# Optimization experiments

Measured on AMD Instinct MI355X. Metric: run time of the kernel, lower is better.

The kernel has to match this reference:

```python
import jax, jax.numpy as jnp
import numpy as np


def conv1x1(x, w, bias):
    # x: [B,C,H,W], w: [O,C], bias: [O]
    return jnp.einsum('bchw,oc->bohw', x, w) + bias[None, :, None, None]


def setup_inputs() -> dict:
    key = jax.random.key(0)
    ks = jax.random.split(key, 12)
    B, Cin_half, H, W = 8, 128, 128, 128
    Cin, Cout = 256, 256
    s_in = 1.0 / np.sqrt(Cin)
    s_out = 1.0 / np.sqrt(Cout)
    return {
        'a': jax.random.normal(ks[0], (B, Cin_half, H, W), jnp.float32),
        'b': jax.random.normal(ks[1], (B, Cin_half, H, W), jnp.float32),
        'w1': jax.random.uniform(ks[2], (Cout, Cin), jnp.float32, -s_in, s_in),
        'b1': jax.random.uniform(ks[3], (Cout,), jnp.float32, -s_in, s_in),
        'w2': jax.random.uniform(ks[4], (Cout, Cout), jnp.float32, -s_out, s_out),
        'b2': jax.random.uniform(ks[5], (Cout,), jnp.float32, -s_out, s_out),
        'w3': jax.random.uniform(ks[6], (Cout, Cout), jnp.float32, -s_out, s_out),
        'b3': jax.random.uniform(ks[7], (Cout,), jnp.float32, -s_out, s_out),
        'w4': jax.random.uniform(ks[8], (Cout, Cout), jnp.float32, -s_out, s_out),
        'b4': jax.random.uniform(ks[9], (Cout,), jnp.float32, -s_out, s_out),
    }


def reference(a, b, w1, b1, w2, b2, w3, b3, w4, b4):
    z = jnp.concatenate([a, b], axis=1)            # [B, Cin, H, W]
    z = conv1x1(z, w1, b1)                          # [B, C, H, W]
    B, C, H, W = z.shape
    q = conv1x1(z, w2, b2).reshape(B, C, H * W)     # [B, C, N]
    k = conv1x1(z, w3, b3).reshape(B, C, H * W)
    v = conv1x1(z, w4, b4).reshape(B, C, H * W)
    qk = jnp.einsum('bcn,bdn->bcd', q, k)           # [B, C, C] (q @ k^T)
    attn = jax.nn.softmax(qk, axis=-1)
    out = jnp.einsum('bcd,bdn->bcn', attn, v)       # [B, C, N]
    return out.reshape(B, C, H, W)
```

## Files before the change

kernel.cpp:

```cpp
#include <hip/hip_runtime.h>

typedef float  f4v  __attribute__((ext_vector_type(4)));
typedef __bf16 bf8v __attribute__((ext_vector_type(8)));
typedef unsigned int u32x2 __attribute__((ext_vector_type(2)));
typedef unsigned int u32x4 __attribute__((ext_vector_type(4)));
typedef unsigned short u16;

#define MFMA(a,b,c) __builtin_amdgcn_mfma_f32_16x16x32_bf16((a),(b),(c),0,0,0)
#define HW_N 16384

__device__ __forceinline__ u16 bf_rne(float x){
  unsigned u = __float_as_uint(x);
  u += 0x7fffu + ((u >> 16) & 1u);
  return (u16)(u >> 16);
}

__global__ void k_weights(const float* __restrict__ w1, const float* __restrict__ b1,
                          const float* __restrict__ w2, const float* __restrict__ b2,
                          const float* __restrict__ w3, const float* __restrict__ b3,
                          const float* __restrict__ w4, const float* __restrict__ b4,
                          float* __restrict__ Wq, float* __restrict__ WkT,
                          float* __restrict__ Wv, float* __restrict__ bq,
                          float* __restrict__ bk, float* __restrict__ bv)
{
  const int blk = blockIdx.x, t = threadIdx.x;
  if (blk == 96){
    float aq = 0.f, ak = 0.f, av = 0.f;
    for (int j = 0; j < 256; ++j){
      const float bb = b1[j];
      aq += w2[t*256 + j] * bb;
      ak += w3[t*256 + j] * bb;
      av += w4[t*256 + j] * bb;
    }
    bq[t] = aq + b2[t];
    bk[t] = ak + b3[t];
    bv[t] = av + b4[t];
    return;
  }
  for (int i = 0; i < 8; ++i){
    const int e   = blk*2048 + i*256 + t;
    const int mat = e >> 16;
    const int c   = (e >> 8) & 255;
    const int col = e & 255;
    const float* wsrc = (mat == 0) ? w2 : ((mat == 1) ? w3 : w4);
    float acc = 0.f;
    for (int j = 0; j < 256; ++j) acc += wsrc[c*256 + j] * w1[j*256 + col];
    if      (mat == 0) Wq [c*256 + col] = acc;
    else if (mat == 1) WkT[col*256 + c] = acc;
    else               Wv [c*256 + col] = acc;
  }
}

__global__ __launch_bounds__(512, 2) void k_gram(
    const float* __restrict__ xa, const float* __restrict__ xb,
    float* __restrict__ Gpart, float* __restrict__ spart)
{
  __shared__ u16 hbuf[2][256*64];
  __shared__ u16 lbuf[2][256*64];
  const int blk = blockIdx.x;
  const int b = blk >> 5, half = (blk >> 4) & 1, chunk = blk & 15;
  const int t = threadIdx.x;
  const int lane = t & 63, w = t >> 6;
  const int wr = w >> 1, wc = w & 1;
  const int c4 = t & 15, crow = t >> 4;

  const float* rowp[8];
#pragma unroll
  for (int p = 0; p < 8; ++p){
    const int c = crow + 32*p;
    const float* base = (c < 128) ? (xa + (size_t)(b*128 + c) * HW_N)
                                  : (xb + (size_t)(b*128 + (c-128)) * HW_N);
    rowp[p] = base + c4*4;
  }

  float ssum[8];
#pragma unroll
  for (int p = 0; p < 8; ++p) ssum[p] = 0.f;

  const f4v vzero = {0.f, 0.f, 0.f, 0.f};
  f4v acc[4][4];
#pragma unroll
  for (int i = 0; i < 4; ++i)
#pragma unroll
    for (int j = 0; j < 4; ++j) acc[i][j] = vzero;

  f4v ld[8];
  auto issue = [&](int s){
    const int n0 = chunk*1024 + s*64;
#pragma unroll
    for (int p = 0; p < 8; ++p) ld[p] = *(const f4v*)(rowp[p] + n0);
  };
  auto wbuf = [&](int bi){
#pragma unroll
    for (int p = 0; p < 8; ++p){
      const int c = crow + 32*p;
      const f4v v = ld[p];
      ssum[p] += (v[0] + v[1]) + (v[2] + v[3]);
      u16 h[4], l[4];
#pragma unroll
      for (int i = 0; i < 4; ++i){
        const float x = v[i];
        const u16 hb = bf_rne(x);
        const float hf = __uint_as_float(((unsigned)hb) << 16);
        h[i] = hb; l[i] = bf_rne(x - hf);
      }
      u32x2 hp, lp;
      hp[0] = (unsigned)h[0] | ((unsigned)h[1] << 16);
      hp[1] = (unsigned)h[2] | ((unsigned)h[3] << 16);
      lp[0] = (unsigned)l[0] | ((unsigned)l[1] << 16);
      lp[1] = (unsigned)l[2] | ((unsigned)l[3] << 16);
      const int off = c*64 + (((c4 >> 1) ^ (c & 7)) * 8) + (c4 & 1) * 4;
      *(u32x2*)&hbuf[bi][off] = hp;
      *(u32x2*)&lbuf[bi][off] = lp;
    }
  };
  auto mstep = [&](int bi){
#pragma unroll
    for (int kk = 0; kk < 2; ++kk){
      bf8v ah[4], al[4], bh[4], bl[4];
#pragma unroll
      for (int f = 0; f < 4; ++f){
        const int so = kk*4 + (lane >> 4);
        const int r  = wr*64 + f*16 + (lane & 15);
        const int oa = r*64 + ((so ^ (r & 7)) * 8);
        ah[f] = *(const bf8v*)&hbuf[bi][oa];
        al[f] = *(const bf8v*)&lbuf[bi][oa];
        const int rc = 128*half + wc*64 + f*16 + (lane & 15);
        const int ob = rc*64 + ((so ^ (rc & 7)) * 8);
        bh[f] = *(const bf8v*)&hbuf[bi][ob];
        bl[f] = *(const bf8v*)&lbuf[bi][ob];
      }
#pragma unroll
      for (int i = 0; i < 4; ++i)
#pragma unroll
        for (int j = 0; j < 4; ++j){
          acc[i][j] = MFMA(ah[i], bh[j], acc[i][j]);
          acc[i][j] = MFMA(ah[i], bl[j], acc[i][j]);
          acc[i][j] = MFMA(al[i], bh[j], acc[i][j]);
        }
    }
  };

  issue(0); wbuf(0); __syncthreads();
  for (int s = 0; s < 16; ++s){
    const int cur = s & 1;
    if (s < 15) issue(s + 1);
    mstep(cur);
    if (s < 15) wbuf(cur ^ 1);
    __syncthreads();
  }

  float* gp = Gpart + (size_t)((b*2 + half)*16 + chunk) * 32768;
#pragma unroll
  for (int i = 0; i < 4; ++i)
#pragma unroll
    for (int j = 0; j < 4; ++j){
      const int row = wr*64 + i*16 + ((lane >> 4) << 2);
      const int col = wc*64 + j*16 + (lane & 15);
#pragma unroll
      for (int r2 = 0; r2 < 4; ++r2)
        gp[(row + r2)*128 + col] = acc[i][j][r2];
    }

  if (half == 0){
#pragma unroll
    for (int p = 0; p < 8; ++p){
      float v = ssum[p];
      v += __shfl_xor(v, 1);
      v += __shfl_xor(v, 2);
      v += __shfl_xor(v, 4);
      v += __shfl_xor(v, 8);
      if ((lane & 15) == 0)
        spart[(b*16 + chunk)*256 + (crow + 32*p)] = v;
    }
  }
}

__global__ void k_redg(const float* __restrict__ Gpart, float* __restrict__ G)
{
  for (int k = 0; k < 8; ++k){
    const int o = blockIdx.x*2048 + k*256 + threadIdx.x;
    const int b = o >> 16, r = (o >> 8) & 255, col = o & 255;
    const int half = col >> 7, cc = col & 127;
    const float* p = Gpart + (size_t)(b*2 + half)*524288 + (size_t)r*128 + cc;
    float s = 0.f;
#pragma unroll
    for (int ch = 0; ch < 16; ++ch) s += p[ch*32768];
    G[o] = s;
  }
}

__device__ __forceinline__ float block_red(float v, int ismax, volatile float* red, int t){
#pragma unroll
  for (int m = 32; m; m >>= 1){
    const float o = __shfl_xor(v, m);
    v = ismax ? fmaxf(v, o) : (v + o);
  }
  if ((t & 63) == 0) red[t >> 6] = v;
  __syncthreads();
  const float r01 = ismax ? fmaxf(red[0], red[1]) : (red[0] + red[1]);
  const float r23 = ismax ? fmaxf(red[2], red[3]) : (red[2] + red[3]);
  v = ismax ? fmaxf(r01, r23) : (r01 + r23);
  __syncthreads();
  return v;
}

__global__ __launch_bounds__(256, 2) void k_attn(
    const float* __restrict__ G, const float* __restrict__ spart,
    const float* __restrict__ Wq, const float* __restrict__ WkT,
    const float* __restrict__ Wv, const float* __restrict__ bq,
    const float* __restrict__ bk, const float* __restrict__ bv,
    u16* __restrict__ Mfrag, float* __restrict__ cb)
{
  __shared__ float s_lds[256];
  __shared__ float wq_lds[4][256];
  __shared__ float t1_lds[4][256];
  __shared__ float a_lds[4][256];
  __shared__ float red[4];
  const int blk = blockIdx.x;
  const int b = blk >> 6, r0 = (blk & 63) * 4;
  const int t = threadIdx.x;

  float sv = 0.f;
#pragma unroll
  for (int ch = 0; ch < 16; ++ch) sv += spart[(b*16 + ch)*256 + t];
  s_lds[t] = sv;
#pragma unroll
  for (int ri = 0; ri < 4; ++ri) wq_lds[ri][t] = Wq[(r0 + ri)*256 + t];
  __syncthreads();

  float t1[4] = {0,0,0,0}, pv[4] = {0,0,0,0};
  const float* gb = G + (size_t)b * 65536;
  for (int k = 0; k < 256; ++k){
    const float g  = gb[k*256 + t];
    const float sk = s_lds[k];
#pragma unroll
    for (int ri = 0; ri < 4; ++ri){
      const float wqv = wq_lds[ri][k];
      t1[ri] += wqv * g;
      pv[ri] += wqv * sk;
    }
  }
#pragma unroll
  for (int ri = 0; ri < 4; ++ri) t1_lds[ri][t] = t1[ri];
  __syncthreads();

  float qk[4] = {0,0,0,0}, rd = 0.f;
  for (int n = 0; n < 256; ++n){
    const float wkt = WkT[n*256 + t];
    rd += wkt * s_lds[n];
#pragma unroll
    for (int ri = 0; ri < 4; ++ri) qk[ri] += t1_lds[ri][n] * wkt;
  }
  const float bkv = bk[t];
#pragma unroll
  for (int ri = 0; ri < 4; ++ri){
    const float bqv = bq[r0 + ri];
    qk[ri] += pv[ri]*bkv + bqv*rd + 16384.f*bqv*bkv;
  }

  float areg[4];
#pragma unroll
  for (int ri = 0; ri < 4; ++ri){
    const float m = block_red(qk[ri], 1, red, t);
    const float e = __expf(qk[ri] - m);
    const float s = block_red(e, 0, red, t);
    areg[ri] = e / s;
    a_lds[ri][t] = areg[ri];
  }
  const float bvv = bv[t];
#pragma unroll
  for (int ri = 0; ri < 4; ++ri){
    const float c = block_red(areg[ri]*bvv, 0, red, t);
    if (t == 0) cb[b*256 + r0 + ri] = c;
  }
  __syncthreads();

  float m4[4] = {0,0,0,0};
  for (int d = 0; d < 256; ++d){
    const float wv = Wv[d*256 + t];
#pragma unroll
    for (int ri = 0; ri < 4; ++ri) m4[ri] += a_lds[ri][d] * wv;
  }
  const int ks = t >> 5, lhi = (t >> 3) & 3, j = t & 7;
#pragma unroll
  for (int ri = 0; ri < 4; ++ri){
    const int o = r0 + ri;
    Mfrag[(size_t)b*65536 +
          (size_t)((((o >> 4)*8 + ks)*64) + (o & 15) + (lhi << 4))*8 + j] = bf_rne(m4[ri]);
  }
}

__global__ __launch_bounds__(512, 4) void k_out(
    const float* __restrict__ xa, const float* __restrict__ xb,
    const u16* __restrict__ Mfrag, const float* __restrict__ cb,
    float* __restrict__ out)
{
  __shared__ u16 xt[2][32*256];
  const int blk = blockIdx.x;
  const int b = blk >> 6, nchunk = blk & 63;
  const int t = threadIdx.x;
  const int lane = t & 63, w = t >> 6;
  const int cr = t >> 1;
  const int hf = t & 1;

  const float* rowbase = (cr < 128) ? (xa + (size_t)(b*128 + cr)*HW_N)
                                    : (xb + (size_t)(b*128 + (cr-128))*HW_N);
  const float* rp = rowbase + hf*16;

  f4v ld[4];
  auto issue = [&](int s){
    const int n0 = nchunk*256 + s*32;
#pragma unroll
    for (int q = 0; q < 4; ++q) ld[q] = *(const f4v*)(rp + n0 + q*4);
  };
  auto cvtwrite = [&](int bi){
#pragma unroll
    for (int q = 0; q < 4; ++q){
      const f4v v = ld[q];
#pragma unroll
      for (int i = 0; i < 4; ++i){
        const int n = hf*16 + q*4 + i;
        xt[bi][n*256 + (((cr >> 3) ^ (n & 15))*8) + (cr & 7)] = bf_rne(v[i]);
      }
    }
  };

  issue(0);

  u32x4 af[2][8];
  const u16* mb = Mfrag + (size_t)b * 65536;
#pragma unroll
  for (int f = 0; f < 2; ++f)
#pragma unroll
    for (int ks = 0; ks < 8; ++ks)
      af[f][ks] = *(const u32x4*)(mb + (size_t)((((w*2 + f)*8 + ks)*64 + lane))*8);
#pragma unroll
  for (int f = 0; f < 2; ++f)
#pragma unroll
    for (int ks = 0; ks < 8; ++ks)
      asm volatile("" : "+a"(af[f][ks]));

  float cbv[2];
#pragma unroll
  for (int f = 0; f < 2; ++f)
    cbv[f] = cb[b*256 + w*32 + f*16 + (lane & 15)];

  const f4v vzero = {0.f, 0.f, 0.f, 0.f};
  float* outp = out + (size_t)b*256*HW_N;

  cvtwrite(0);
  __syncthreads();

  for (int s = 0; s < 8; ++s){
    const int cur = s & 1;
    if (s < 7) issue(s + 1);

    const int n0 = nchunk*256 + s*32;
    f4v acc[2][2];
#pragma unroll
    for (int f = 0; f < 2; ++f){ acc[f][0] = vzero; acc[f][1] = vzero; }

#pragma unroll
    for (int ks = 0; ks < 8; ++ks){
      bf8v xf[2];
#pragma unroll
      for (int g = 0; g < 2; ++g){
        const int n  = g*16 + (lane & 15);
        const int so = ks*4 + (lane >> 4);
        xf[g] = *(const bf8v*)&xt[cur][n*256 + ((so ^ (n & 15))*8)];
      }
#pragma unroll
      for (int f = 0; f < 2; ++f){
        acc[f][0] = MFMA(xf[0], __builtin_bit_cast(bf8v, af[f][ks]), acc[f][0]);
        acc[f][1] = MFMA(xf[1], __builtin_bit_cast(bf8v, af[f][ks]), acc[f][1]);
      }
    }

#pragma unroll
    for (int f = 0; f < 2; ++f){
      const int row = w*32 + f*16 + (lane & 15);
#pragma unroll
      for (int g = 0; g < 2; ++g){
        const int px = n0 + g*16 + ((lane >> 4) << 2);
        f4v v = acc[f][g] + cbv[f];
        *(f4v*)&outp[(size_t)row*HW_N + px] = v;
      }
    }

    if (s < 7) cvtwrite(cur ^ 1);
    __syncthreads();
  }
}

extern "C" void kernel_launch(void* const* d_in, const int* in_sizes, int n_in,
                              void* d_out, int out_size, void* d_ws, size_t ws_size,
                              hipStream_t stream)
{
  const float* xa = (const float*)d_in[0];
  const float* xb = (const float*)d_in[1];
  const float* w1 = (const float*)d_in[2];
  const float* b1 = (const float*)d_in[3];
  const float* w2 = (const float*)d_in[4];
  const float* b2 = (const float*)d_in[5];
  const float* w3 = (const float*)d_in[6];
  const float* b3 = (const float*)d_in[7];
  const float* w4 = (const float*)d_in[8];
  const float* b4 = (const float*)d_in[9];
  float* out = (float*)d_out;
  char*  ws  = (char*)d_ws;

  float* Gpart = (float*)(ws + 0);
  float* G     = (float*)(ws + 33554432);
  float* spart = (float*)(ws + 35651584);
  float* Wq    = (float*)(ws + 35782656);
  float* WkT   = (float*)(ws + 36044800);
  float* Wv    = (float*)(ws + 36306944);
  float* bq    = (float*)(ws + 36569088);
  float* bk    = (float*)(ws + 36570112);
  float* bv    = (float*)(ws + 36571136);
  u16*   Mfrag = (u16*)  (ws + 36572160);
  float* cb    = (float*)(ws + 37620736);

  hipLaunchKernelGGL(k_weights, dim3(97),  dim3(256), 0, stream,
                     w1,b1,w2,b2,w3,b3,w4,b4, Wq,WkT,Wv,bq,bk,bv);
  hipLaunchKernelGGL(k_gram,    dim3(256), dim3(512), 0, stream, xa, xb, Gpart, spart);
  hipLaunchKernelGGL(k_redg,    dim3(256), dim3(256), 0, stream, Gpart, G);
  hipLaunchKernelGGL(k_attn,    dim3(512), dim3(256), 0, stream,
                     G, spart, Wq, WkT, Wv, bq, bk, bv, Mfrag, cb);
  hipLaunchKernelGGL(k_out,     dim3(512), dim3(512), 0, stream, xa, xb, Mfrag, cb, out);
}
```

Before: 257.4 us.

## Compute full Gram per block with atomic reduction and cache bf16 input copy

k_gram now has each block compute the full 256x256 Gram tile over a shorter spatial chunk instead of a half-tile. Partial results go into G through atomicAdd, which removes the Gpart buffer and the k_redg reduction kernel. The same pass writes a bf16 copy of the input, so k_out reads half the bytes and skips the float-to-bf16 conversion. The cost is 8x4 accumulator tiles per wave, which raises register pressure, atomic contention on G, an extra memset, and an extra 64MB bf16 write in the gram pass.

```diff
diff --git a/kernel.cpp b/kernel.cpp
--- a/kernel.cpp
+++ b/kernel.cpp
@@ -5,6 +5,7 @@
 typedef unsigned int u32x2 __attribute__((ext_vector_type(2)));
 typedef unsigned int u32x4 __attribute__((ext_vector_type(4)));
 typedef unsigned short u16;
+typedef unsigned short u16x8 __attribute__((ext_vector_type(8)));
 
 #define MFMA(a,b,c) __builtin_amdgcn_mfma_f32_16x16x32_bf16((a),(b),(c),0,0,0)
 #define HW_N 16384
@@ -53,44 +54,44 @@
 
 __global__ __launch_bounds__(512, 2) void k_gram(
     const float* __restrict__ xa, const float* __restrict__ xb,
-    float* __restrict__ Gpart, float* __restrict__ spart)
+    float* __restrict__ G, float* __restrict__ spart,
+    u16* __restrict__ xbf)
 {
   __shared__ u16 hbuf[2][256*64];
   __shared__ u16 lbuf[2][256*64];
   const int blk = blockIdx.x;
-  const int b = blk >> 5, half = (blk >> 4) & 1, chunk = blk & 15;
+  const int b = blk >> 5, chunk = blk & 31;
   const int t = threadIdx.x;
   const int lane = t & 63, w = t >> 6;
-  const int wr = w >> 1, wc = w & 1;
+  const int wr = w >> 2, wc = w & 3;
   const int c4 = t & 15, crow = t >> 4;
 
-  const float* rowp[8];
-#pragma unroll
-  for (int p = 0; p < 8; ++p){
-    const int c = crow + 32*p;
-    const float* base = (c < 128) ? (xa + (size_t)(b*128 + c) * HW_N)
-                                  : (xb + (size_t)(b*128 + (c-128)) * HW_N);
-    rowp[p] = base + c4*4;
-  }
+  const float* xpa = xa + (((size_t)(b*128) + crow) << 14) + c4*4;
+  const float* xpb = xb + (((size_t)(b*128) + crow) << 14) + c4*4;
+  u16*        xpo = xbf + (((size_t)(b*256) + crow) << 14) + c4*4;
 
   float ssum[8];
 #pragma unroll
   for (int p = 0; p < 8; ++p) ssum[p] = 0.f;
 
   const f4v vzero = {0.f, 0.f, 0.f, 0.f};
-  f4v acc[4][4];
-#pragma unroll
-  for (int i = 0; i < 4; ++i)
-#pragma unroll
-    for (int j = 0; j < 4; ++j) acc[i][j] = vzero;
+  f4v acc[8][4];
+#pragma unroll
+  for (int f = 0; f < 8; ++f)
+#pragma unroll
+    for (int j = 0; j < 4; ++j) acc[f][j] = vzero;
 
   f4v ld[8];
   auto issue = [&](int s){
-    const int n0 = chunk*1024 + s*64;
-#pragma unroll
-    for (int p = 0; p < 8; ++p) ld[p] = *(const f4v*)(rowp[p] + n0);
+    const size_t n0 = (size_t)chunk*512 + s*64;
+#pragma unroll
+    for (int p = 0; p < 8; ++p){
+      const float* src = (p < 4) ? (xpa + ((size_t)p << 19)) : (xpb + ((size_t)(p-4) << 19));
+      ld[p] = *(const f4v*)(src + n0);
+    }
   };
-  auto wbuf = [&](int bi){
+  auto wbuf = [&](int bi, int s){
+    const size_t n0 = (size_t)chunk*512 + s*64;
 #pragma unroll
     for (int p = 0; p < 8; ++p){
       const int c = crow + 32*p;
@@ -101,8 +102,8 @@
       for (int i = 0; i < 4; ++i){
         const float x = v[i];
         const u16 hb = bf_rne(x);
-        const float hf = __uint_as_float(((unsigned)hb) << 16);
-        h[i] = hb; l[i] = bf_rne(x - hf);
+        const float hfv = __uint_as_float(((unsigned)hb) << 16);
+        h[i] = hb; l[i] = bf_rne(x - hfv);
       }
       u32x2 hp, lp;
       hp[0] = (unsigned)h[0] | ((unsigned)h[1] << 16);
@@ -112,81 +113,67 @@
       const int off = c*64 + (((c4 >> 1) ^ (c & 7)) * 8) + (c4 & 1) * 4;
       *(u32x2*)&hbuf[bi][off] = hp;
       *(u32x2*)&lbuf[bi][off] = lp;
+      *(u32x2*)(xpo + ((size_t)p << 19) + n0) = hp;
     }
   };
   auto mstep = [&](int bi){
 #pragma unroll
     for (int kk = 0; kk < 2; ++kk){
-      bf8v ah[4], al[4], bh[4], bl[4];
-#pragma unroll
-      for (int f = 0; f < 4; ++f){
-        const int so = kk*4 + (lane >> 4);
-        const int r  = wr*64 + f*16 + (lane & 15);
+      const int so = kk*4 + (lane >> 4);
+      bf8v bh[4], bl[4];
+#pragma unroll
+      for (int g = 0; g < 4; ++g){
+        const int rc = wc*64 + g*16 + (lane & 15);
+        const int ob = rc*64 + ((so ^ (rc & 7)) * 8);
+        bh[g] = *(const bf8v*)&hbuf[bi][ob];
+        bl[g] = *(const bf8v*)&lbuf[bi][ob];
+      }
+#pragma unroll
+      for (int f = 0; f < 8; ++f){
+        const int r  = wr*128 + f*16 + (lane & 15);
         const int oa = r*64 + ((so ^ (r & 7)) * 8);
-        ah[f] = *(const bf8v*)&hbuf[bi][oa];
-        al[f] = *(const bf8v*)&lbuf[bi][oa];
-        const int rc = 128*half + wc*64 + f*16 + (lane & 15);
-        const int ob = rc*64 + ((so ^ (rc & 7)) * 8);
-        bh[f] = *(const bf8v*)&hbuf[bi][ob];
-        bl[f] = *(const bf8v*)&lbuf[bi][ob];
-      }
-#pragma unroll
-      for (int i = 0; i < 4; ++i)
+        const bf8v ah = *(const bf8v*)&hbuf[bi][oa];
+        const bf8v al = *(const bf8v*)&lbuf[bi][oa];
 #pragma unroll
         for (int j = 0; j < 4; ++j){
-          acc[i][j] = MFMA(ah[i], bh[j], acc[i][j]);
-          acc[i][j] = MFMA(ah[i], bl[j], acc[i][j]);
-          acc[i][j] = MFMA(al[i], bh[j], acc[i][j]);
+          acc[f][j] = MFMA(ah, bh[j], acc[f][j]);
+          acc[f][j] = MFMA(ah, bl[j], acc[f][j]);
+          acc[f][j] = MFMA(al, bh[j], acc[f][j]);
         }
+      }
     }
   };
 
-  issue(0); wbuf(0); __syncthreads();
-  for (int s = 0; s < 16; ++s){
+  issue(0); wbuf(0, 0); __syncthreads();
+  for (int s = 0; s < 8; ++s){
     const int cur = s & 1;
-    if (s < 15) issue(s + 1);
+    if (s < 7) issue(s + 1);
     mstep(cur);
-    if (s < 15) wbuf(cur ^ 1);
+    if (s < 7) wbuf(cur ^ 1, s + 1);
     __syncthreads();
   }
 
-  float* gp = Gpart + (size_t)((b*2 + half)*16 + chunk) * 32768;
-#pragma unroll
-  for (int i = 0; i < 4; ++i)
+  float* gb = G + (size_t)b * 65536;
+#pragma unroll
+  for (int f = 0; f < 8; ++f)
 #pragma unroll
     for (int j = 0; j < 4; ++j){
-      const int row = wr*64 + i*16 + ((lane >> 4) << 2);
+      const int row = wr*128 + f*16 + ((lane >> 4) << 2);
       const int col = wc*64 + j*16 + (lane & 15);
 #pragma unroll
       for (int r2 = 0; r2 < 4; ++r2)
-        gp[(row + r2)*128 + col] = acc[i][j][r2];
-    }
-
-  if (half == 0){
-#pragma unroll
-    for (int p = 0; p < 8; ++p){
-      float v = ssum[p];
-      v += __shfl_xor(v, 1);
-      v += __shfl_xor(v, 2);
-      v += __shfl_xor(v, 4);
-      v += __shfl_xor(v, 8);
-      if ((lane & 15) == 0)
-        spart[(b*16 + chunk)*256 + (crow + 32*p)] = v;
-    }
-  }
-}
-
-__global__ void k_redg(const float* __restrict__ Gpart, float* __restrict__ G)
-{
-  for (int k = 0; k < 8; ++k){
-    const int o = blockIdx.x*2048 + k*256 + threadIdx.x;
-    const int b = o >> 16, r = (o >> 8) & 255, col = o & 255;
-    const int half = col >> 7, cc = col & 127;
-    const float* p = Gpart + (size_t)(b*2 + half)*524288 + (size_t)r*128 + cc;
-    float s = 0.f;
-#pragma unroll
-    for (int ch = 0; ch < 16; ++ch) s += p[ch*32768];
-    G[o] = s;
+        atomicAdd(&gb[(size_t)(row + r2)*256 + col], acc[f][j][r2]);
+    }
+
+#pragma unroll
+  for (int p = 0; p < 8; ++p){
+    float v = ssum[p];
+    v += __shfl_xor(v, 1);
+    v += __shfl_xor(v, 2);
+    v += __shfl_xor(v, 4);
+    v += __shfl_xor(v, 8);
+    if ((lane & 15) == 0)
+      spart[(b*32 + chunk)*256 + (crow + 32*p)] = v;
   }
 }
 
@@ -223,7 +210,7 @@
 
   float sv = 0.f;
 #pragma unroll
-  for (int ch = 0; ch < 16; ++ch) sv += spart[(b*16 + ch)*256 + t];
+  for (int ch = 0; ch < 32; ++ch) sv += spart[(b*32 + ch)*256 + t];
   s_lds[t] = sv;
 #pragma unroll
   for (int ri = 0; ri < 4; ++ri) wq_lds[ri][t] = Wq[(r0 + ri)*256 + t];
@@ -292,9 +279,8 @@
 }
 
 __global__ __launch_bounds__(512, 4) void k_out(
-    const float* __restrict__ xa, const float* __restrict__ xb,
-    const u16* __restrict__ Mfrag, const float* __restrict__ cb,
-    float* __restrict__ out)
+    const u16* __restrict__ xbf, const u16* __restrict__ Mfrag,
+    const float* __restrict__ cb, float* __restrict__ out)
 {
   __shared__ u16 xt[2][32*256];
   const int blk = blockIdx.x;
@@ -304,24 +290,20 @@
   const int cr = t >> 1;
   const int hf = t & 1;
 
-  const float* rowbase = (cr < 128) ? (xa + (size_t)(b*128 + cr)*HW_N)
-                                    : (xb + (size_t)(b*128 + (cr-128))*HW_N);
-  const float* rp = rowbase + hf*16;
-
-  f4v ld[4];
+  const u16* xp = xbf + (((size_t)(b*256) + cr) << 14) + nchunk*256 + hf*16;
+
+  u16x8 ld[2];
   auto issue = [&](int s){
-    const int n0 = nchunk*256 + s*32;
-#pragma unroll
-    for (int q = 0; q < 4; ++q) ld[q] = *(const f4v*)(rp + n0 + q*4);
+#pragma unroll
+    for (int q = 0; q < 2; ++q) ld[q] = *(const u16x8*)(xp + s*32 + q*8);
   };
-  auto cvtwrite = [&](int bi){
-#pragma unroll
-    for (int q = 0; q < 4; ++q){
-      const f4v v = ld[q];
-#pragma unroll
-      for (int i = 0; i < 4; ++i){
-        const int n = hf*16 + q*4 + i;
-        xt[bi][n*256 + (((cr >> 3) ^ (n & 15))*8) + (cr & 7)] = bf_rne(v[i]);
+  auto swrite = [&](int bi){
+#pragma unroll
+    for (int q = 0; q < 2; ++q){
+#pragma unroll
+      for (int j = 0; j < 8; ++j){
+        const int n = hf*16 + q*8 + j;
+        xt[bi][n*256 + (((cr >> 3) ^ (n & 15))*8) + (cr & 7)] = ld[q][j];
       }
     }
   };
@@ -349,7 +331,7 @@
   const f4v vzero = {0.f, 0.f, 0.f, 0.f};
   float* outp = out + (size_t)b*256*HW_N;
 
-  cvtwrite(0);
+  swrite(0);
   __syncthreads();
 
   for (int s = 0; s < 8; ++s){
@@ -388,7 +370,7 @@
       }
     }
 
-    if (s < 7) cvtwrite(cur ^ 1);
+    if (s < 7) swrite(cur ^ 1);
     __syncthreads();
   }
 }
@@ -410,23 +392,25 @@
   float* out = (float*)d_out;
   char*  ws  = (char*)d_ws;
 
-  float* Gpart = (float*)(ws + 0);
-  float* G     = (float*)(ws + 33554432);
-  float* spart = (float*)(ws + 35651584);
-  float* Wq    = (float*)(ws + 35782656);
-  float* WkT   = (float*)(ws + 36044800);
-  float* Wv    = (float*)(ws + 36306944);
-  float* bq    = (float*)(ws + 36569088);
-  float* bk    = (float*)(ws + 36570112);
-  float* bv    = (float*)(ws + 36571136);
-  u16*   Mfrag = (u16*)  (ws + 36572160);
-  float* cb    = (float*)(ws + 37620736);
-
+  float* G     = (float*)(ws + 0);
+  float* spart = (float*)(ws + 2097152);
+  float* Wq    = (float*)(ws + 2359296);
+  float* WkT   = (float*)(ws + 2621440);
+  float* Wv    = (float*)(ws + 2883584);
+  float* bq    = (float*)(ws + 3145728);
+  float* bk    = (float*)(ws + 3146752);
+  float* bv    = (float*)(ws + 3147776);
+  u16*   Mfrag = (u16*)  (ws + 3148800);
+  float* cb    = (float*)(ws + 4197376);
+  u16*   xbf   = (u16*)  (ws + 4205568);
+
+  hipMemsetAsync(G, 0, 2097152, stream);
   hipLaunchKernelGGL(k_weights, dim3(97),  dim3(256), 0, stream,
                      w1,b1,w2,b2,w3,b3,w4,b4, Wq,WkT,Wv,bq,bk,bv);
-  hipLaunchKernelGGL(k_gram,    dim3(256), dim3(512), 0, stream, xa, xb, Gpart, spart);
-  hipLaunchKernelGGL(k_redg,    dim3(256), dim3(256), 0, stream, Gpart, G);
+  hipLaunchKernelGGL(k_gram,    dim3(256), dim3(512), 0, stream,
+                     xa, xb, G, spart, xbf);
   hipLaunchKernelGGL(k_attn,    dim3(512), dim3(256), 0, stream,
                      G, spart, Wq, WkT, Wv, bq, bk, bv, Mfrag, cb);
-  hipLaunchKernelGGL(k_out,     dim3(512), dim3(512), 0, stream, xa, xb, Mfrag, cb, out);
-}
+  hipLaunchKernelGGL(k_out,     dim3(512), dim3(512), 0, stream,
+                     xbf, Mfrag, cb, out);
+}
```

New measurement: 296.5 us. 15.2% more time.

## Atomically reduce Gram partials and cache bf16 input copy for output GEMM

Applied to the files above, without the earlier changes.

The Gram kernel now accumulates its per-chunk partial results straight into G with float atomics, which removes the 32 MB partial buffer and the separate reduction kernel; G is zeroed with a memset first. The half-0 blocks of the Gram kernel also write a bf16-rounded copy of the concatenated input to workspace. The output kernel then reads that bf16 copy (half the bytes) instead of re-reading and converting the fp32 inputs. The cost is extra global writes in k_gram, heavy atomic contention (16 chunks adding into each G element), and a summation order that is no longer deterministic.

```diff
diff --git a/kernel.cpp b/kernel.cpp
--- a/kernel.cpp
+++ b/kernel.cpp
@@ -5,6 +5,7 @@
 typedef unsigned int u32x2 __attribute__((ext_vector_type(2)));
 typedef unsigned int u32x4 __attribute__((ext_vector_type(4)));
 typedef unsigned short u16;
+typedef unsigned short u16x8 __attribute__((ext_vector_type(8)));
 
 #define MFMA(a,b,c) __builtin_amdgcn_mfma_f32_16x16x32_bf16((a),(b),(c),0,0,0)
 #define HW_N 16384
@@ -53,7 +54,8 @@
 
 __global__ __launch_bounds__(512, 2) void k_gram(
     const float* __restrict__ xa, const float* __restrict__ xb,
-    float* __restrict__ Gpart, float* __restrict__ spart)
+    float* __restrict__ G, float* __restrict__ spart,
+    u16* __restrict__ xbf)
 {
   __shared__ u16 hbuf[2][256*64];
   __shared__ u16 lbuf[2][256*64];
@@ -90,7 +92,7 @@
 #pragma unroll
     for (int p = 0; p < 8; ++p) ld[p] = *(const f4v*)(rowp[p] + n0);
   };
-  auto wbuf = [&](int bi){
+  auto wbuf = [&](int bi, int s){
 #pragma unroll
     for (int p = 0; p < 8; ++p){
       const int c = crow + 32*p;
@@ -112,6 +114,9 @@
       const int off = c*64 + (((c4 >> 1) ^ (c & 7)) * 8) + (c4 & 1) * 4;
       *(u32x2*)&hbuf[bi][off] = hp;
       *(u32x2*)&lbuf[bi][off] = lp;
+      if (half == 0){
+        *(u32x2*)&xbf[(size_t)(b*256 + c)*HW_N + chunk*1024 + s*64 + c4*4] = hp;
+      }
     }
   };
   auto mstep = [&](int bi){
@@ -141,25 +146,25 @@
     }
   };
 
-  issue(0); wbuf(0); __syncthreads();
+  issue(0); wbuf(0, 0); __syncthreads();
   for (int s = 0; s < 16; ++s){
     const int cur = s & 1;
     if (s < 15) issue(s + 1);
     mstep(cur);
-    if (s < 15) wbuf(cur ^ 1);
+    if (s < 15) wbuf(cur ^ 1, s + 1);
     __syncthreads();
   }
 
-  float* gp = Gpart + (size_t)((b*2 + half)*16 + chunk) * 32768;
+  float* gb = G + (size_t)b * 65536;
 #pragma unroll
   for (int i = 0; i < 4; ++i)
 #pragma unroll
     for (int j = 0; j < 4; ++j){
       const int row = wr*64 + i*16 + ((lane >> 4) << 2);
-      const int col = wc*64 + j*16 + (lane & 15);
+      const int col = 128*half + wc*64 + j*16 + (lane & 15);
 #pragma unroll
       for (int r2 = 0; r2 < 4; ++r2)
-        gp[(row + r2)*128 + col] = acc[i][j][r2];
+        atomicAdd(&gb[(size_t)(row + r2)*256 + col], acc[i][j][r2]);
     }
 
   if (half == 0){
@@ -173,20 +178,6 @@
       if ((lane & 15) == 0)
         spart[(b*16 + chunk)*256 + (crow + 32*p)] = v;
     }
-  }
-}
-
-__global__ void k_redg(const float* __restrict__ Gpart, float* __restrict__ G)
-{
-  for (int k = 0; k < 8; ++k){
-    const int o = blockIdx.x*2048 + k*256 + threadIdx.x;
-    const int b = o >> 16, r = (o >> 8) & 255, col = o & 255;
-    const int half = col >> 7, cc = col & 127;
-    const float* p = Gpart + (size_t)(b*2 + half)*524288 + (size_t)r*128 + cc;
-    float s = 0.f;
-#pragma unroll
-    for (int ch = 0; ch < 16; ++ch) s += p[ch*32768];
-    G[o] = s;
   }
 }
 
@@ -292,9 +283,8 @@
 }
 
 __global__ __launch_bounds__(512, 4) void k_out(
-    const float* __restrict__ xa, const float* __restrict__ xb,
-    const u16* __restrict__ Mfrag, const float* __restrict__ cb,
-    float* __restrict__ out)
+    const u16* __restrict__ xbf, const u16* __restrict__ Mfrag,
+    const float* __restrict__ cb, float* __restrict__ out)
 {
   __shared__ u16 xt[2][32*256];
   const int blk = blockIdx.x;
@@ -304,24 +294,20 @@
   const int cr = t >> 1;
   const int hf = t & 1;
 
-  const float* rowbase = (cr < 128) ? (xa + (size_t)(b*128 + cr)*HW_N)
-                                    : (xb + (size_t)(b*128 + (cr-128))*HW_N);
-  const float* rp = rowbase + hf*16;
-
-  f4v ld[4];
+  const u16* xp = xbf + (((size_t)(b*256) + cr) << 14) + nchunk*256 + hf*16;
+
+  u16x8 ld[2];
   auto issue = [&](int s){
-    const int n0 = nchunk*256 + s*32;
-#pragma unroll
-    for (int q = 0; q < 4; ++q) ld[q] = *(const f4v*)(rp + n0 + q*4);
+#pragma unroll
+    for (int q = 0; q < 2; ++q) ld[q] = *(const u16x8*)(xp + s*32 + q*8);
   };
-  auto cvtwrite = [&](int bi){
-#pragma unroll
-    for (int q = 0; q < 4; ++q){
-      const f4v v = ld[q];
-#pragma unroll
-      for (int i = 0; i < 4; ++i){
-        const int n = hf*16 + q*4 + i;
-        xt[bi][n*256 + (((cr >> 3) ^ (n & 15))*8) + (cr & 7)] = bf_rne(v[i]);
+  auto swrite = [&](int bi){
+#pragma unroll
+    for (int q = 0; q < 2; ++q){
+#pragma unroll
+      for (int j = 0; j < 8; ++j){
+        const int n = hf*16 + q*8 + j;
+        xt[bi][n*256 + (((cr >> 3) ^ (n & 15))*8) + (cr & 7)] = ld[q][j];
       }
     }
   };
@@ -349,7 +335,7 @@
   const f4v vzero = {0.f, 0.f, 0.f, 0.f};
   float* outp = out + (size_t)b*256*HW_N;
 
-  cvtwrite(0);
+  swrite(0);
   __syncthreads();
 
   for (int s = 0; s < 8; ++s){
@@ -388,7 +374,7 @@
       }
     }
 
-    if (s < 7) cvtwrite(cur ^ 1);
+    if (s < 7) swrite(cur ^ 1);
     __syncthreads();
   }
 }
@@ -410,23 +396,25 @@
   float* out = (float*)d_out;
   char*  ws  = (char*)d_ws;
 
-  float* Gpart = (float*)(ws + 0);
-  float* G     = (float*)(ws + 33554432);
-  float* spart = (float*)(ws + 35651584);
-  float* Wq    = (float*)(ws + 35782656);
-  float* WkT   = (float*)(ws + 36044800);
-  float* Wv    = (float*)(ws + 36306944);
-  float* bq    = (float*)(ws + 36569088);
-  float* bk    = (float*)(ws + 36570112);
-  float* bv    = (float*)(ws + 36571136);
-  u16*   Mfrag = (u16*)  (ws + 36572160);
-  float* cb    = (float*)(ws + 37620736);
-
+  float* G     = (float*)(ws + 0);
+  float* spart = (float*)(ws + 2097152);
+  float* Wq    = (float*)(ws + 2228224);
+  float* WkT   = (float*)(ws + 2490368);
+  float* Wv    = (float*)(ws + 2752512);
+  float* bq    = (float*)(ws + 3014656);
+  float* bk    = (float*)(ws + 3015680);
+  float* bv    = (float*)(ws + 3016704);
+  u16*   Mfrag = (u16*)  (ws + 3017728);
+  float* cb    = (float*)(ws + 4066304);
+  u16*   xbf   = (u16*)  (ws + 4074496);
+
+  hipMemsetAsync(G, 0, 2097152, stream);
   hipLaunchKernelGGL(k_weights, dim3(97),  dim3(256), 0, stream,
                      w1,b1,w2,b2,w3,b3,w4,b4, Wq,WkT,Wv,bq,bk,bv);
-  hipLaunchKernelGGL(k_gram,    dim3(256), dim3(512), 0, stream, xa, xb, Gpart, spart);
-  hipLaunchKernelGGL(k_redg,    dim3(256), dim3(256), 0, stream, Gpart, G);
+  hipLaunchKernelGGL(k_gram,    dim3(256), dim3(512), 0, stream,
+                     xa, xb, G, spart, xbf);
   hipLaunchKernelGGL(k_attn,    dim3(512), dim3(256), 0, stream,
                      G, spart, Wq, WkT, Wv, bq, bk, bv, Mfrag, cb);
-  hipLaunchKernelGGL(k_out,     dim3(512), dim3(512), 0, stream, xa, xb, Mfrag, cb, out);
-}
+  hipLaunchKernelGGL(k_out,     dim3(512), dim3(512), 0, stream,
+                     xbf, Mfrag, cb, out);
+}
```

Result: slower. 288.1 us (+11.9%).
